# Kernel tuning notes

Hardware: AMD Instinct MI355X
Metric: run time of the kernel (lower is better)

Reference implementation:

```python
import jax, jax.numpy as jnp
import numpy as np

B, N, NF, C = 1, 5000, 10000, 128   # batch, vertices, faces, feature width
LAYERS = 30
NNZ = 48 * B * NF  # ~3 verts/face * 16 entries per 4x4 quaternion block


def spmm(rows, cols, vals, x, n_rows):
    # sparse COO [n_rows, n_cols] @ dense x [n_cols, d] -> [n_rows, d]
    return jax.ops.segment_sum(vals[:, None] * x[cols], rows, num_segments=n_rows)


def graph_bn(x, gamma, beta, eps=1e-5):
    # GraphBatchNorm: BatchNorm1d over (batch, nodes) per channel, training-mode stats
    mean = jnp.mean(x, axis=(0, 1))
    var = jnp.var(x, axis=(0, 1))
    return gamma * (x - mean) * jax.lax.rsqrt(var + eps) + beta


def gc_pre(x, gamma, beta, W, b):
    # GraphConv1x1 with batch_norm='pre'
    return graph_bn(x, gamma, beta) @ W + b


def _forward(inputs, mask, Di_rows, Di_cols, Di_vals, DiA_rows, DiA_cols, DiA_vals,
             W_in, b_in, g0, be0, W0, b0, g1, be1, Wl1, bl1, g2, be2, W_out, b_out):
    Bv, Nv, _ = inputs.shape
    v = inputs @ W_in + b_in                      # conv1 (batch_norm=None)
    f = jnp.zeros((Bv, NF, C), inputs.dtype)      # face features start at zero
    for i in range(LAYERS):
        if i % 2 == 0:
            # DirResNet2: Dirac operator message passing vertices<->faces
            x_in, f_in = jax.nn.elu(v), jax.nn.elu(f)
            # vertices -> faces; C channels viewed as 4 quaternion components x C//4
            Dv = spmm(Di_rows, Di_cols, Di_vals,
                      x_in.reshape(Bv * Nv * 4, C // 4), 4 * Bv * NF).reshape(Bv, NF, C)
            f_out = gc_pre(jnp.concatenate([f_in, Dv], -1), g0[i], be0[i], W0[i], b0[i])
            # adjoint Dirac: faces -> vertices
            DAf = spmm(DiA_rows, DiA_cols, DiA_vals,
                       jax.nn.elu(f_out).reshape(Bv * NF * 4, C // 4), 4 * Bv * Nv).reshape(Bv, Nv, C)
            v = v + gc_pre(jnp.concatenate([x_in, DAf], -1), g1[i], be1[i], Wl1[i], bl1[i])
            f = f_out
        else:
            # AvgResNet2: masked global average pooling block
            x = v
            for (g, be, W, b) in ((g0[i], be0[i], W0[i], b0[i]),
                                  (g1[i], be1[i], Wl1[i], bl1[i])):
                x = jax.nn.elu(x)
                avg = jnp.sum(x * mask, axis=1, keepdims=True) / jnp.sum(mask, axis=1, keepdims=True)
                x = jnp.concatenate([x, jnp.broadcast_to(avg, x.shape)], -1)
                x = gc_pre(x, g, be, W, b)
            v = x + v
    out = gc_pre(v, g2, be2, W_out, b_out)        # conv2 (batch_norm='pre')
    return jax.nn.elu(out)


def setup_inputs():
    key = jax.random.key(0)
    ks = jax.random.split(key, 12)
    return {
        "inputs": jax.random.normal(ks[0], (B, N, 3), jnp.float32),
        "mask": jnp.ones((B, N, 1), jnp.float32),
        "Di_rows": jax.random.randint(ks[1], (NNZ,), 0, 4 * B * NF, jnp.int32),
        "Di_cols": jax.random.randint(ks[2], (NNZ,), 0, 4 * B * N, jnp.int32),
        "Di_vals": jax.random.normal(ks[3], (NNZ,), jnp.float32),
        "DiA_rows": jax.random.randint(ks[4], (NNZ,), 0, 4 * B * N, jnp.int32),
        "DiA_cols": jax.random.randint(ks[5], (NNZ,), 0, 4 * B * NF, jnp.int32),
        "DiA_vals": jax.random.normal(ks[6], (NNZ,), jnp.float32),
        "W_in": jax.random.normal(ks[7], (3, C), jnp.float32) * 0.5,
        "b_in": jnp.zeros((C,), jnp.float32),
        "g0": jnp.ones((LAYERS, 2 * C), jnp.float32),
        "be0": jnp.zeros((LAYERS, 2 * C), jnp.float32),
        "W0": jax.random.normal(ks[8], (LAYERS, 2 * C, C), jnp.float32) * 0.05,
        "b0": jnp.zeros((LAYERS, C), jnp.float32),
        "g1": jnp.ones((LAYERS, 2 * C), jnp.float32),
        "be1": jnp.zeros((LAYERS, 2 * C), jnp.float32),
        "Wl1": jax.random.normal(ks[9], (LAYERS, 2 * C, C), jnp.float32) * 0.05,
        "bl1": jnp.zeros((LAYERS, C), jnp.float32),
        "g2": jnp.ones((C,), jnp.float32),
        "be2": jnp.zeros((C,), jnp.float32),
        "W_out": jax.random.normal(ks[10], (C, 1), jnp.float32) * 0.1,
        "b_out": jnp.zeros((1,), jnp.float32),
    }


def reference(inputs, mask, Di_rows, Di_cols, Di_vals, DiA_rows, DiA_cols, DiA_vals,
              W_in, b_in, g0, be0, W0, b0, g1, be1, Wl1, bl1, g2, be2, W_out, b_out):
    return _forward(inputs, mask, Di_rows, Di_cols, Di_vals, DiA_rows, DiA_cols, DiA_vals,
                    W_in, b_in, g0, be0, W0, b0, g1, be1, Wl1, bl1, g2, be2, W_out, b_out)
```

## Files before the change

### kernel.cpp

```cpp
#include <hip/hip_runtime.h>
#include <math.h>

#define N_V 5000
#define N_F 10000
#define NNZ 480000
#define LAYERS 30
#define STC 4096

typedef short short8 __attribute__((ext_vector_type(8)));
typedef float f32x4 __attribute__((ext_vector_type(4)));
union BFu { uint4 u; short8 s8; short s[8]; unsigned short us[8]; };

__device__ __forceinline__ float eluf(float x){ return x>0.f ? x : expm1f(x); }
__device__ __forceinline__ unsigned short f2bf(float f){
  unsigned u = __float_as_uint(f);
  unsigned r = (u + 0x7fffu + ((u>>16)&1u)) >> 16;
  return (unsigned short)r;
}
__device__ __forceinline__ float bf2f(unsigned short u){
  return __uint_as_float((unsigned)u << 16);
}

__global__ void hist_both(const int* __restrict__ Di_rows, const int* __restrict__ DiA_rows,
                          int* __restrict__ Di_cur, int* __restrict__ DA_cur){
  int e = blockIdx.x*256 + threadIdx.x;
  if(e < NNZ){
    atomicAdd(&Di_cur[Di_rows[e]], 1);
    atomicAdd(&DA_cur[DiA_rows[e]], 1);
  }
}

__global__ void chunkscan(const int* __restrict__ Di_cur, int* __restrict__ Di_ptr,
                          const int* __restrict__ DA_cur, int* __restrict__ DA_ptr,
                          int* __restrict__ bsumDi, int* __restrict__ bsumDA){
  __shared__ int ish[256];
  int b = blockIdx.x, tid = threadIdx.x;
  const int nchDi = 157;
  const int* hist; int* optr; int n; int cb; int* bs;
  if(b < nchDi){ hist=Di_cur; optr=Di_ptr; n=40000; cb=b; bs=bsumDi; }
  else { hist=DA_cur; optr=DA_ptr; n=20000; cb=b-nchDi; bs=bsumDA; }
  int i = cb*256 + tid;
  int v = (i<n)? hist[i] : 0;
  ish[tid]=v; __syncthreads();
  for(int off=1; off<256; off<<=1){
    int t = (tid>=off)? ish[tid-off] : 0;
    __syncthreads(); ish[tid]+=t; __syncthreads();
  }
  if(i<n) optr[i] = ish[tid]-v;
  if(tid==255) bs[cb]=ish[255];
}

__global__ void topscan(int* __restrict__ bsumDi, int* __restrict__ bsumDA){
  __shared__ int ish[256];
  int tid=threadIdx.x;
  int* bs = (blockIdx.x==0) ? bsumDi : bsumDA;
  int n  = (blockIdx.x==0) ? 157 : 79;
  int v = (tid<n)? bs[tid] : 0;
  ish[tid]=v; __syncthreads();
  for(int off=1; off<256; off<<=1){
    int t=(tid>=off)? ish[tid-off]:0;
    __syncthreads(); ish[tid]+=t; __syncthreads();
  }
  if(tid<n) bs[tid]=ish[tid]-v;
}

__global__ void addback(int* __restrict__ Di_ptr, int* __restrict__ Di_cur,
                        const int* __restrict__ bsumDi,
                        int* __restrict__ DA_ptr, int* __restrict__ DA_cur,
                        const int* __restrict__ bsumDA){
  int stride = gridDim.x*256;
  int base = blockIdx.x*256 + threadIdx.x;
  for(int i=base;i<40000;i+=stride){ int v=Di_ptr[i]+bsumDi[i>>8]; Di_ptr[i]=v; Di_cur[i]=v; }
  for(int i=base;i<20000;i+=stride){ int v=DA_ptr[i]+bsumDA[i>>8]; DA_ptr[i]=v; DA_cur[i]=v; }
  if(base==0){ Di_ptr[40000]=NNZ; DA_ptr[20000]=NNZ; }
}

__global__ void scatter_pairs(const int* __restrict__ Di_rows, int* __restrict__ Di_cur,
                              const int* __restrict__ Di_cols, const float* __restrict__ Di_vals,
                              float2* __restrict__ Di_pairs,
                              const int* __restrict__ DiA_rows, int* __restrict__ DA_cur,
                              const int* __restrict__ DiA_cols, const float* __restrict__ DiA_vals,
                              float2* __restrict__ DA_pairs){
  int g = blockIdx.x & 7;
  int sub = blockIdx.x >> 3;
  int lo_di = g*5000, hi_di = lo_di+5000;
  int lo_da = g*2500, hi_da = lo_da+2500;
  int stride = (gridDim.x>>3)*256;
  for(int e = sub*256 + threadIdx.x; e < NNZ; e += stride){
    int r = Di_rows[e];
    if(r >= lo_di && r < hi_di){
      int pos = atomicAdd(&Di_cur[r], 1);
      Di_pairs[pos] = make_float2(__int_as_float(Di_cols[e]), Di_vals[e]);
    }
    r = DiA_rows[e];
    if(r >= lo_da && r < hi_da){
      int pos = atomicAdd(&DA_cur[r], 1);
      DA_pairs[pos] = make_float2(__int_as_float(DiA_cols[e]), DiA_vals[e]);
    }
  }
}

__global__ void wconv(const float* __restrict__ W0, const float* __restrict__ Wl1,
                      unsigned short* __restrict__ Wt){
  __shared__ float tile[32][129];
  int b  = blockIdx.x >> 3;
  int kt = blockIdx.x & 7;
  int i = b>>1, m = b&1;
  const float* W = (m ? Wl1 : W0) + (size_t)i*32768;
  unsigned short* out = Wt + (size_t)b*32768;
  int tid = threadIdx.x;
  int n = tid & 127, kr = tid >> 7;
  for(int kk = kr; kk < 32; kk += 2)
    tile[kk][n] = W[(kt*32 + kk)*128 + n];
  __syncthreads();
  int kp = tid & 31, n8 = tid >> 5;
  for(int nn = n8; nn < 128; nn += 8)
    out[nn*256 + kt*32 + kp] = f2bf(tile[kp][nn]);
}

__global__ void conv1_kernel(const float* __restrict__ in, const float* __restrict__ W_in,
                             const float* __restrict__ b_in,
                             const float* __restrict__ be0, const float* __restrict__ be1,
                             const unsigned short* __restrict__ Wt,
                             float* __restrict__ v_raw, unsigned short* __restrict__ elu_v,
                             float* __restrict__ st1, float* __restrict__ oddb){
  __shared__ float pool[256];
  int tid = threadIdx.x;
  int stride = gridDim.x*256;
  int cpy = (blockIdx.x&7)*512;
  float ls=0.f, ls2=0.f;
  for(int idx = blockIdx.x*256+tid; idx < N_V*128; idx += stride){
    int n = idx>>7, c = idx&127;
    float v = b_in[c] + in[n*3]*W_in[c] + in[n*3+1]*W_in[128+c] + in[n*3+2]*W_in[256+c];
    v_raw[idx] = v;
    float ev = eluf(v);
    elu_v[idx] = f2bf(ev);
    ls += ev; ls2 += ev*ev;
  }
  int ch = tid & 127;
  pool[tid]=ls; __syncthreads();
  if(tid<128) atomicAdd(&st1[cpy+ch], pool[tid]+pool[tid+128]);
  __syncthreads();
  pool[tid]=ls2; __syncthreads();
  if(tid<128) atomicAdd(&st1[cpy+256+ch], pool[tid]+pool[tid+128]);
  for(int item = blockIdx.x*256+tid; item < LAYERS*2*128; item += stride){
    int b = item >> 7;
    int i = b >> 1, m = b & 1;
    int j = item & 127;
    const float* bp = (m ? be1 : be0) + i*256 + 128;
    const unsigned short* wp = Wt + (size_t)b*32768 + j*256 + 128;
    float s = 0.f;
    #pragma unroll 8
    for(int k=0;k<128;++k) s += bp[k]*bf2f(wp[k]);
    oddb[item] = s;
  }
}

__global__ __launch_bounds__(256) void spmm_bn(
    const int* __restrict__ ptr, const float2* __restrict__ pairs,
    const unsigned short* __restrict__ x, float* __restrict__ y, int nrows,
    float* __restrict__ stslot){
  __shared__ float pool[512];
  int tid = threadIdx.x;
  int w = tid>>6, lane = tid&63;
  int slot = lane>>3, jg = lane&7;
  int row = blockIdx.x*32 + w*8 + slot;
  float4 acc = make_float4(0,0,0,0);
  if(row < nrows){
    int s0 = ptr[row], e0 = ptr[row+1];
    int last = e0 - 1;
    for(int i = s0; i < e0; i += 4){
      int i1 = min(i+1, last), i2 = min(i+2, last), i3 = min(i+3, last);
      float2 p0 = pairs[i];
      float2 p1 = pairs[i1];
      float2 p2 = pairs[i2];
      float2 p3 = pairs[i3];
      float w1 = (i+1 <= last) ? p1.y : 0.f;
      float w2 = (i+2 <= last) ? p2.y : 0.f;
      float w3 = (i+3 <= last) ? p3.y : 0.f;
      ushort4 x0 = *(const ushort4*)&x[(__float_as_int(p0.x)<<5) + jg*4];
      ushort4 x1 = *(const ushort4*)&x[(__float_as_int(p1.x)<<5) + jg*4];
      ushort4 x2 = *(const ushort4*)&x[(__float_as_int(p2.x)<<5) + jg*4];
      ushort4 x3 = *(const ushort4*)&x[(__float_as_int(p3.x)<<5) + jg*4];
      acc.x += p0.y*bf2f(x0.x) + w1*bf2f(x1.x) + w2*bf2f(x2.x) + w3*bf2f(x3.x);
      acc.y += p0.y*bf2f(x0.y) + w1*bf2f(x1.y) + w2*bf2f(x2.y) + w3*bf2f(x3.y);
      acc.z += p0.y*bf2f(x0.z) + w1*bf2f(x1.z) + w2*bf2f(x2.z) + w3*bf2f(x3.z);
      acc.w += p0.y*bf2f(x0.w) + w1*bf2f(x1.w) + w2*bf2f(x2.w) + w3*bf2f(x3.w);
    }
    *(float4*)&y[(row<<5) + jg*4] = acc;
  }
  float4 ls2 = make_float4(acc.x*acc.x, acc.y*acc.y, acc.z*acc.z, acc.w*acc.w);
  acc.x += __shfl_xor(acc.x, 32); acc.y += __shfl_xor(acc.y, 32);
  acc.z += __shfl_xor(acc.z, 32); acc.w += __shfl_xor(acc.w, 32);
  ls2.x += __shfl_xor(ls2.x, 32); ls2.y += __shfl_xor(ls2.y, 32);
  ls2.z += __shfl_xor(ls2.z, 32); ls2.w += __shfl_xor(ls2.w, 32);
  if(slot < 4) *(float4*)&pool[w*128 + slot*32 + jg*4] = acc;
  __syncthreads();
  int cpy = (blockIdx.x&7)*512;
  if(tid < 128){
    int c = (tid + (blockIdx.x<<3)) & 127;
    atomicAdd(&stslot[cpy+128+c], pool[c]+pool[128+c]+pool[256+c]+pool[384+c]);
  }
  __syncthreads();
  if(slot < 4) *(float4*)&pool[w*128 + slot*32 + jg*4] = ls2;
  __syncthreads();
  if(tid < 128){
    int c = (tid + (blockIdx.x<<3)) & 127;
    atomicAdd(&stslot[cpy+384+c], pool[c]+pool[128+c]+pool[256+c]+pool[384+c]);
  }
}

__global__ __launch_bounds__(256) void gemm_mfma(
    const unsigned short* __restrict__ A0, const float* __restrict__ A1,
    const float* __restrict__ st, float invM,
    const float* __restrict__ g, const float* __restrict__ be,
    const unsigned short* __restrict__ Wt, const float* __restrict__ bias,
    const float* __restrict__ bias2, const float* __restrict__ resid,
    float* __restrict__ out_raw, unsigned short* __restrict__ out_elu,
    float* __restrict__ stE, float* __restrict__ stR, int M, int K)
{
  __shared__ float ab[256], bb[256];
  int tid = threadIdx.x;
  if(tid < K){
    float s1 = 0.f, s2v = 0.f;
    #pragma unroll
    for(int c8=0;c8<8;++c8){ s1 += st[c8*512 + tid]; s2v += st[c8*512 + 256 + tid]; }
    float mean = s1*invM;
    float var  = fmaxf(s2v*invM - mean*mean, 0.f);
    float aa   = g[tid]*rsqrtf(var + 1e-5f);
    ab[tid] = aa; bb[tid] = be[tid] - mean*aa;
  }
  __syncthreads();

  int wave = tid>>6, lane = tid&63;
  int ln = lane&15, q = lane>>4;
  int r0 = blockIdx.x*16;
  int c0 = wave*32;
  int kq = q*8;
  int arow = r0 + ln;
  bool aok = arow < M;

  f32x4 acc[2] = {};
  for(int kb=0; kb<K; kb+=32){
    int kg = kb + kq;
    float av[8];
    if(!aok){
      #pragma unroll
      for(int j2=0;j2<8;++j2) av[j2]=0.f;
    } else if(A1 && kg >= 128){
      int kk = kg - 128;
      float4 x0 = *(const float4*)&A1[arow*128 + kk];
      float4 x1 = *(const float4*)&A1[arow*128 + kk + 4];
      av[0]=x0.x; av[1]=x0.y; av[2]=x0.z; av[3]=x0.w;
      av[4]=x1.x; av[5]=x1.y; av[6]=x1.z; av[7]=x1.w;
    } else {
      BFu raw; raw.u = *(const uint4*)&A0[arow*128 + kg];
      #pragma unroll
      for(int j2=0;j2<8;++j2) av[j2] = bf2f(raw.us[j2]);
    }
    BFu af;
    #pragma unroll
    for(int j2=0;j2<8;++j2) af.us[j2] = f2bf(fmaf(av[j2], ab[kg+j2], bb[kg+j2]));
    #pragma unroll
    for(int nb=0;nb<2;++nb){
      int n = c0 + nb*16 + ln;
      BFu bfv; bfv.u = *(const uint4*)&Wt[n*256 + kb + kq];
      acc[nb] = __builtin_amdgcn_mfma_f32_16x16x32_bf16(af.s8, bfv.s8, acc[nb], 0, 0, 0);
    }
  }

  int rbase = r0 + q*4;
  bool wantR = (stR != nullptr);
  int cpy = (blockIdx.x&7)*512;
  #pragma unroll
  for(int nb=0;nb<2;++nb){
    int col = c0 + nb*16 + ln;
    float bsum = bias[col] + (bias2 ? bias2[col] : 0.f);
    float s=0.f, s2=0.f, rs=0.f, rs2=0.f;
    #pragma unroll
    for(int reg=0;reg<4;++reg){
      int row = rbase + reg;
      bool ok = row < M;
      float v = acc[nb][reg] + bsum;
      if(resid && ok) v += resid[row*128 + col];
      float ve = eluf(v);
      if(ok){
        if(out_raw) out_raw[row*128 + col] = v;
        if(out_elu) out_elu[row*128 + col] = f2bf(ve);
        s += ve; s2 += ve*ve;
        if(wantR){ rs += v; rs2 += v*v; }
      }
    }
    s  += __shfl_xor(s, 16);  s  += __shfl_xor(s, 32);
    s2 += __shfl_xor(s2, 16); s2 += __shfl_xor(s2, 32);
    if(wantR){
      rs  += __shfl_xor(rs, 16);  rs  += __shfl_xor(rs, 32);
      rs2 += __shfl_xor(rs2, 16); rs2 += __shfl_xor(rs2, 32);
    }
    if(q==0){
      if(stE){ atomicAdd(&stE[cpy+col], s); atomicAdd(&stE[cpy+256+col], s2); }
      if(wantR){ atomicAdd(&stR[cpy+col], rs); atomicAdd(&stR[cpy+256+col], rs2); }
    }
  }
}

__global__ void final_kernel(const float* __restrict__ v_raw, const float* __restrict__ st,
                             const float* __restrict__ g2, const float* __restrict__ be2,
                             const float* __restrict__ W_out, const float* __restrict__ b_out,
                             float* __restrict__ out){
  __shared__ float pool[256];
  int tid = threadIdx.x; int half = tid>>7, k = tid&127;
  float s1 = 0.f, s2v = 0.f;
  #pragma unroll
  for(int c8=0;c8<8;++c8){ s1 += st[c8*512 + k]; s2v += st[c8*512 + 256 + k]; }
  float mean = s1*(1.f/N_V);
  float var = fmaxf(s2v*(1.f/N_V) - mean*mean, 0.f);
  float aa = g2[k]*rsqrtf(var+1e-5f);
  float scale = aa*W_out[k];
  float cons = (be2[k]-mean*aa)*W_out[k];
  int r = blockIdx.x*2 + half;
  float val = v_raw[r*128+k]*scale + cons;
  pool[tid]=val; __syncthreads();
  for(int s=64;s>=1;s>>=1){ if(k<s) pool[tid]+=pool[tid+s]; __syncthreads(); }
  if(k==0) out[r] = eluf(pool[tid] + b_out[0]);
}

extern "C" void kernel_launch(void* const* d_in, const int* in_sizes, int n_in,
                              void* d_out, int out_size, void* d_ws, size_t ws_size,
                              hipStream_t stream){
  const float* inputs  = (const float*)d_in[0];
  const int*   Di_rows = (const int*)d_in[2];
  const int*   Di_cols = (const int*)d_in[3];
  const float* Di_vals = (const float*)d_in[4];
  const int*   DiA_rows= (const int*)d_in[5];
  const int*   DiA_cols= (const int*)d_in[6];
  const float* DiA_vals= (const float*)d_in[7];
  const float* W_in = (const float*)d_in[8];  const float* b_in = (const float*)d_in[9];
  const float* g0  = (const float*)d_in[10];  const float* be0 = (const float*)d_in[11];
  const float* W0  = (const float*)d_in[12];  const float* b0  = (const float*)d_in[13];
  const float* g1  = (const float*)d_in[14];  const float* be1 = (const float*)d_in[15];
  const float* Wl1 = (const float*)d_in[16];  const float* bl1 = (const float*)d_in[17];
  const float* g2  = (const float*)d_in[18];  const float* be2 = (const float*)d_in[19];
  const float* W_out = (const float*)d_in[20]; const float* b_out = (const float*)d_in[21];

  float* ws = (float*)d_ws;
  float* v_raw = ws;
  unsigned short* elu_v0 = (unsigned short*)(ws + 640000);
  unsigned short* elu_v1 = (unsigned short*)(ws + 960000);
  unsigned short* elu_f0 = (unsigned short*)(ws + 1280000);
  float* Dv    = ws + 2560000;
  float* DAf   = ws + 3840000;
  float* st    = ws + 4480000;
  float* oddb  = ws + 4742144;
  int* Di_ptr  = (int*)(ws + 4749824);
  int* DA_ptr  = (int*)(ws + 4789825);
  int* Di_cur  = (int*)(ws + 4809826);
  int* DA_cur  = (int*)(ws + 4849826);
  float2* Di_pairs = (float2*)(ws + 4869826);
  float2* DA_pairs = (float2*)(ws + 5829826);
  int* bsumDi  = (int*)(ws + 6789826);
  int* bsumDA  = (int*)(ws + 6790082);
  unsigned short* Wt = (unsigned short*)(ws + 6790212);
  unsigned short* elu_f1 = (unsigned short*)(ws + 7773252);
  unsigned short* elu_x1 = (unsigned short*)Dv;

  unsigned short* Vb[2] = {elu_v0, elu_v1};
  unsigned short* Fb[2] = {elu_f0, elu_f1};

  hipMemsetAsync(st, 0, (size_t)64*STC*sizeof(float), stream);
  hipMemsetAsync(elu_f0, 0, (size_t)1280000*sizeof(unsigned short), stream);
  hipMemsetAsync(Di_cur, 0, (size_t)60000*sizeof(int), stream);

  hist_both<<<1875, 256, 0, stream>>>(Di_rows, DiA_rows, Di_cur, DA_cur);
  chunkscan<<<236, 256, 0, stream>>>(Di_cur, Di_ptr, DA_cur, DA_ptr, bsumDi, bsumDA);
  topscan<<<2, 256, 0, stream>>>(bsumDi, bsumDA);
  addback<<<236, 256, 0, stream>>>(Di_ptr, Di_cur, bsumDi, DA_ptr, DA_cur, bsumDA);
  scatter_pairs<<<2048, 256, 0, stream>>>(Di_rows, Di_cur, Di_cols, Di_vals, Di_pairs,
                                          DiA_rows, DA_cur, DiA_cols, DiA_vals, DA_pairs);
  wconv<<<480, 256, 0, stream>>>(W0, Wl1, Wt);
  conv1_kernel<<<640, 256, 0, stream>>>(inputs, W_in, b_in, be0, be1, Wt,
                                        v_raw, elu_v0, st + STC, oddb);

  int pv = 0, pf = 0;
  for(int i=0;i<LAYERS;++i){
    if((i&1)==0){
      float* S0  = st + (size_t)(2*i)*STC;
      float* S1b = st + (size_t)(2*i+1)*STC;
      spmm_bn<<<1250, 256, 0, stream>>>(Di_ptr, Di_pairs, Vb[pv], Dv, 40000, S0);
      gemm_mfma<<<625, 256, 0, stream>>>(Fb[pf], Dv, S0, 1.f/N_F, g0+i*256, be0+i*256,
                                         Wt + (size_t)(2*i)*32768, b0+i*128, nullptr,
                                         nullptr, nullptr, Fb[pf^1],
                                         st+(size_t)(2*(i+2))*STC, nullptr, N_F, 256);
      pf ^= 1;
      spmm_bn<<<625, 256, 0, stream>>>(DA_ptr, DA_pairs, Fb[pf], DAf, 20000, S1b);
      gemm_mfma<<<313, 256, 0, stream>>>(Vb[pv], DAf, S1b, 1.f/N_V, g1+i*256, be1+i*256,
                                         Wt + (size_t)(2*i+1)*32768, bl1+i*128, nullptr,
                                         v_raw, v_raw, Vb[pv^1],
                                         st+(size_t)(2*(i+1))*STC, nullptr, N_V, 256);
      pv ^= 1;
    } else {
      float* S0  = st + (size_t)(2*i)*STC;
      float* S1b = st + (size_t)(2*i+1)*STC;
      gemm_mfma<<<313, 256, 0, stream>>>(Vb[pv], nullptr, S0, 1.f/N_V, g0+i*256, be0+i*256,
                                         Wt + (size_t)(2*i)*32768, b0+i*128, oddb+i*256,
                                         nullptr, nullptr, elu_x1,
                                         S1b, nullptr, N_V, 128);
      float* stE = (i==LAYERS-1) ? nullptr : st+(size_t)(2*i+3)*STC;
      float* stR = (i==LAYERS-1) ? st+(size_t)62*STC : nullptr;
      gemm_mfma<<<313, 256, 0, stream>>>(elu_x1, nullptr, S1b, 1.f/N_V, g1+i*256, be1+i*256,
                                         Wt + (size_t)(2*i+1)*32768, bl1+i*128, oddb+i*256+128,
                                         v_raw, v_raw, Vb[pv],
                                         stE, stR, N_V, 128);
    }
  }
  final_kernel<<<2500, 256, 0, stream>>>(v_raw, st+(size_t)62*STC, g2, be2, W_out, b_out,
                                         (float*)d_out);
}
```

Baseline: 1.262 ms.

## Fuse odd-layer GEMM pair with grid barrier; privatize edge histogram

The two back-to-back GEMM launches of each AvgResNet block become one persistent kernel. It keeps the first GEMM's ELU output tile in shared memory and uses a global atomic grid barrier to wait for the batch-norm statistics before running the second GEMM. This removes 15 kernel launches and a global round trip for the intermediate activation. The risk is that the barrier requires all 313 blocks to be co-resident, otherwise it can deadlock. Separately, the edge histogram now uses 8 privatized copies to reduce atomic contention, and the scan sums those copies.

```diff
diff --git a/kernel.cpp b/kernel.cpp
--- a/kernel.cpp
+++ b/kernel.cpp
@@ -22,25 +22,30 @@
 }
 
 __global__ void hist_both(const int* __restrict__ Di_rows, const int* __restrict__ DiA_rows,
-                          int* __restrict__ Di_cur, int* __restrict__ DA_cur){
+                          int* __restrict__ Di_hist, int* __restrict__ DA_hist){
   int e = blockIdx.x*256 + threadIdx.x;
+  int c = blockIdx.x & 7;
   if(e < NNZ){
-    atomicAdd(&Di_cur[Di_rows[e]], 1);
-    atomicAdd(&DA_cur[DiA_rows[e]], 1);
-  }
-}
-
-__global__ void chunkscan(const int* __restrict__ Di_cur, int* __restrict__ Di_ptr,
-                          const int* __restrict__ DA_cur, int* __restrict__ DA_ptr,
+    atomicAdd(&Di_hist[c*40000 + Di_rows[e]], 1);
+    atomicAdd(&DA_hist[c*20000 + DiA_rows[e]], 1);
+  }
+}
+
+__global__ void chunkscan(const int* __restrict__ Di_hist, int* __restrict__ Di_ptr,
+                          const int* __restrict__ DA_hist, int* __restrict__ DA_ptr,
                           int* __restrict__ bsumDi, int* __restrict__ bsumDA){
   __shared__ int ish[256];
   int b = blockIdx.x, tid = threadIdx.x;
   const int nchDi = 157;
   const int* hist; int* optr; int n; int cb; int* bs;
-  if(b < nchDi){ hist=Di_cur; optr=Di_ptr; n=40000; cb=b; bs=bsumDi; }
-  else { hist=DA_cur; optr=DA_ptr; n=20000; cb=b-nchDi; bs=bsumDA; }
+  if(b < nchDi){ hist=Di_hist; optr=Di_ptr; n=40000; cb=b; bs=bsumDi; }
+  else { hist=DA_hist; optr=DA_ptr; n=20000; cb=b-nchDi; bs=bsumDA; }
   int i = cb*256 + tid;
-  int v = (i<n)? hist[i] : 0;
+  int v = 0;
+  if(i<n){
+    #pragma unroll
+    for(int c8=0;c8<8;++c8) v += hist[c8*n + i];
+  }
   ish[tid]=v; __syncthreads();
   for(int off=1; off<256; off<<=1){
     int t = (tid>=off)? ish[tid-off] : 0;
@@ -304,6 +309,152 @@
   }
 }
 
+__global__ __launch_bounds__(256,2) void odd_fused(
+    unsigned short* __restrict__ xelu,
+    const float* __restrict__ st0,
+    const float* __restrict__ g0v, const float* __restrict__ be0v,
+    const unsigned short* __restrict__ Wt0, const float* __restrict__ b0v,
+    const float* __restrict__ ob0,
+    const float* __restrict__ g1v, const float* __restrict__ be1v,
+    const unsigned short* __restrict__ Wt1, const float* __restrict__ b1v,
+    const float* __restrict__ ob1,
+    float* __restrict__ v_raw,
+    float* __restrict__ st1, float* __restrict__ stE, float* __restrict__ stR,
+    int* __restrict__ bar, int nblk)
+{
+  __shared__ float ab[128], bb[128];
+  __shared__ unsigned short x1s[16][136];
+  int tid = threadIdx.x;
+  if(tid < 128){
+    float s1 = 0.f, s2v = 0.f;
+    #pragma unroll
+    for(int c8=0;c8<8;++c8){ s1 += st0[c8*512 + tid]; s2v += st0[c8*512 + 256 + tid]; }
+    float mean = s1*(1.f/N_V);
+    float var  = fmaxf(s2v*(1.f/N_V) - mean*mean, 0.f);
+    float aa   = g0v[tid]*rsqrtf(var + 1e-5f);
+    ab[tid] = aa; bb[tid] = be0v[tid] - mean*aa;
+  }
+  __syncthreads();
+
+  int wave = tid>>6, lane = tid&63;
+  int ln = lane&15, q = lane>>4;
+  int r0 = blockIdx.x*16;
+  int c0 = wave*32;
+  int kq = q*8;
+  int arow = r0 + ln;
+  bool aok = arow < N_V;
+  int cpy = (blockIdx.x&7)*512;
+  int rbase = r0 + q*4;
+
+  f32x4 acc[2] = {};
+  for(int kb=0; kb<128; kb+=32){
+    int kg = kb + kq;
+    BFu raw;
+    if(aok) raw.u = *(const uint4*)&xelu[arow*128 + kg];
+    else    raw.u = make_uint4(0,0,0,0);
+    BFu af;
+    #pragma unroll
+    for(int j2=0;j2<8;++j2) af.us[j2] = f2bf(fmaf(bf2f(raw.us[j2]), ab[kg+j2], bb[kg+j2]));
+    #pragma unroll
+    for(int nb=0;nb<2;++nb){
+      int n = c0 + nb*16 + ln;
+      BFu bfv; bfv.u = *(const uint4*)&Wt0[n*256 + kb + kq];
+      acc[nb] = __builtin_amdgcn_mfma_f32_16x16x32_bf16(af.s8, bfv.s8, acc[nb], 0, 0, 0);
+    }
+  }
+  #pragma unroll
+  for(int nb=0;nb<2;++nb){
+    int col = c0 + nb*16 + ln;
+    float bsum = b0v[col] + ob0[col];
+    float s=0.f, s2=0.f;
+    #pragma unroll
+    for(int reg=0;reg<4;++reg){
+      int row = rbase + reg;
+      float v = acc[nb][reg] + bsum;
+      float ve = eluf(v);
+      x1s[q*4+reg][col] = f2bf(ve);
+      if(row < N_V){ s += ve; s2 += ve*ve; }
+    }
+    s  += __shfl_xor(s, 16);  s  += __shfl_xor(s, 32);
+    s2 += __shfl_xor(s2, 16); s2 += __shfl_xor(s2, 32);
+    if(q==0){ atomicAdd(&st1[cpy+col], s); atomicAdd(&st1[cpy+256+col], s2); }
+  }
+
+  __threadfence();
+  __syncthreads();
+  if(tid==0){
+    __hip_atomic_fetch_add(bar, 1, __ATOMIC_ACQ_REL, __HIP_MEMORY_SCOPE_AGENT);
+    while(__hip_atomic_load(bar, __ATOMIC_ACQUIRE, __HIP_MEMORY_SCOPE_AGENT) < nblk)
+      __builtin_amdgcn_s_sleep(8);
+  }
+  __syncthreads();
+
+  if(tid < 128){
+    float s1 = 0.f, s2v = 0.f;
+    #pragma unroll
+    for(int c8=0;c8<8;++c8){
+      s1  += __hip_atomic_load(&st1[c8*512 + tid],       __ATOMIC_RELAXED, __HIP_MEMORY_SCOPE_AGENT);
+      s2v += __hip_atomic_load(&st1[c8*512 + 256 + tid], __ATOMIC_RELAXED, __HIP_MEMORY_SCOPE_AGENT);
+    }
+    float mean = s1*(1.f/N_V);
+    float var  = fmaxf(s2v*(1.f/N_V) - mean*mean, 0.f);
+    float aa   = g1v[tid]*rsqrtf(var + 1e-5f);
+    ab[tid] = aa; bb[tid] = be1v[tid] - mean*aa;
+  }
+  __syncthreads();
+
+  f32x4 acc2[2] = {};
+  for(int kb=0; kb<128; kb+=32){
+    int kg = kb + kq;
+    ushort4 xa = *(const ushort4*)&x1s[ln][kg];
+    ushort4 xb = *(const ushort4*)&x1s[ln][kg+4];
+    BFu af;
+    af.us[0]=f2bf(fmaf(bf2f(xa.x), ab[kg+0], bb[kg+0]));
+    af.us[1]=f2bf(fmaf(bf2f(xa.y), ab[kg+1], bb[kg+1]));
+    af.us[2]=f2bf(fmaf(bf2f(xa.z), ab[kg+2], bb[kg+2]));
+    af.us[3]=f2bf(fmaf(bf2f(xa.w), ab[kg+3], bb[kg+3]));
+    af.us[4]=f2bf(fmaf(bf2f(xb.x), ab[kg+4], bb[kg+4]));
+    af.us[5]=f2bf(fmaf(bf2f(xb.y), ab[kg+5], bb[kg+5]));
+    af.us[6]=f2bf(fmaf(bf2f(xb.z), ab[kg+6], bb[kg+6]));
+    af.us[7]=f2bf(fmaf(bf2f(xb.w), ab[kg+7], bb[kg+7]));
+    #pragma unroll
+    for(int nb=0;nb<2;++nb){
+      int n = c0 + nb*16 + ln;
+      BFu bfv; bfv.u = *(const uint4*)&Wt1[n*256 + kb + kq];
+      acc2[nb] = __builtin_amdgcn_mfma_f32_16x16x32_bf16(af.s8, bfv.s8, acc2[nb], 0, 0, 0);
+    }
+  }
+  bool wantR = (stR != nullptr);
+  #pragma unroll
+  for(int nb=0;nb<2;++nb){
+    int col = c0 + nb*16 + ln;
+    float bsum = b1v[col] + ob1[col];
+    float s=0.f, s2=0.f, rs=0.f, rs2=0.f;
+    #pragma unroll
+    for(int reg=0;reg<4;++reg){
+      int row = rbase + reg;
+      if(row < N_V){
+        float v = acc2[nb][reg] + bsum + v_raw[row*128 + col];
+        float ve = eluf(v);
+        v_raw[row*128 + col] = v;
+        xelu[row*128 + col] = f2bf(ve);
+        s += ve; s2 += ve*ve;
+        if(wantR){ rs += v; rs2 += v*v; }
+      }
+    }
+    s  += __shfl_xor(s, 16);  s  += __shfl_xor(s, 32);
+    s2 += __shfl_xor(s2, 16); s2 += __shfl_xor(s2, 32);
+    if(wantR){
+      rs  += __shfl_xor(rs, 16);  rs  += __shfl_xor(rs, 32);
+      rs2 += __shfl_xor(rs2, 16); rs2 += __shfl_xor(rs2, 32);
+    }
+    if(q==0){
+      if(stE){ atomicAdd(&stE[cpy+col], s); atomicAdd(&stE[cpy+256+col], s2); }
+      if(wantR){ atomicAdd(&stR[cpy+col], rs); atomicAdd(&stR[cpy+256+col], rs2); }
+    }
+  }
+}
+
 __global__ void final_kernel(const float* __restrict__ v_raw, const float* __restrict__ st,
                              const float* __restrict__ g2, const float* __restrict__ be2,
                              const float* __restrict__ W_out, const float* __restrict__ b_out,
@@ -362,7 +513,9 @@
   int* bsumDA  = (int*)(ws + 6790082);
   unsigned short* Wt = (unsigned short*)(ws + 6790212);
   unsigned short* elu_f1 = (unsigned short*)(ws + 7773252);
-  unsigned short* elu_x1 = (unsigned short*)Dv;
+  int* Di_hist = (int*)Di_pairs;
+  int* DA_hist = (int*)DA_pairs;
+  int* bar     = (int*)(st + (size_t)63*STC);
 
   unsigned short* Vb[2] = {elu_v0, elu_v1};
   unsigned short* Fb[2] = {elu_f0, elu_f1};
@@ -370,9 +523,11 @@
   hipMemsetAsync(st, 0, (size_t)64*STC*sizeof(float), stream);
   hipMemsetAsync(elu_f0, 0, (size_t)1280000*sizeof(unsigned short), stream);
   hipMemsetAsync(Di_cur, 0, (size_t)60000*sizeof(int), stream);
-
-  hist_both<<<1875, 256, 0, stream>>>(Di_rows, DiA_rows, Di_cur, DA_cur);
-  chunkscan<<<236, 256, 0, stream>>>(Di_cur, Di_ptr, DA_cur, DA_ptr, bsumDi, bsumDA);
+  hipMemsetAsync(Di_hist, 0, (size_t)320000*sizeof(int), stream);
+  hipMemsetAsync(DA_hist, 0, (size_t)160000*sizeof(int), stream);
+
+  hist_both<<<1875, 256, 0, stream>>>(Di_rows, DiA_rows, Di_hist, DA_hist);
+  chunkscan<<<236, 256, 0, stream>>>(Di_hist, Di_ptr, DA_hist, DA_ptr, bsumDi, bsumDA);
   topscan<<<2, 256, 0, stream>>>(bsumDi, bsumDA);
   addback<<<236, 256, 0, stream>>>(Di_ptr, Di_cur, bsumDi, DA_ptr, DA_cur, bsumDA);
   scatter_pairs<<<2048, 256, 0, stream>>>(Di_rows, Di_cur, Di_cols, Di_vals, Di_pairs,
@@ -401,16 +556,15 @@
     } else {
       float* S0  = st + (size_t)(2*i)*STC;
       float* S1b = st + (size_t)(2*i+1)*STC;
-      gemm_mfma<<<313, 256, 0, stream>>>(Vb[pv], nullptr, S0, 1.f/N_V, g0+i*256, be0+i*256,
-                                         Wt + (size_t)(2*i)*32768, b0+i*128, oddb+i*256,
-                                         nullptr, nullptr, elu_x1,
-                                         S1b, nullptr, N_V, 128);
       float* stE = (i==LAYERS-1) ? nullptr : st+(size_t)(2*i+3)*STC;
       float* stR = (i==LAYERS-1) ? st+(size_t)62*STC : nullptr;
-      gemm_mfma<<<313, 256, 0, stream>>>(elu_x1, nullptr, S1b, 1.f/N_V, g1+i*256, be1+i*256,
-                                         Wt + (size_t)(2*i+1)*32768, bl1+i*128, oddb+i*256+128,
-                                         v_raw, v_raw, Vb[pv],
-                                         stE, stR, N_V, 128);
+      odd_fused<<<313, 256, 0, stream>>>(Vb[pv], S0,
+                                         g0+i*256, be0+i*256, Wt + (size_t)(2*i)*32768,
+                                         b0+i*128, oddb+i*256,
+                                         g1+i*256, be1+i*256, Wt + (size_t)(2*i+1)*32768,
+                                         bl1+i*128, oddb+i*256+128,
+                                         v_raw, S1b, stE, stR,
+                                         bar + (i>>1), 313);
     }
   }
   final_kernel<<<2500, 256, 0, stream>>>(v_raw, st+(size_t)62*STC, g2, be2, W_out, b_out,
```

Result: slower. 1.847 ms (+46.4%).
